# Kernel tuning notes

Measured on AMD Instinct MI355X. Metric: run time of the kernel, lower is better.

## Reference

```python
import jax, jax.numpy as jnp
import numpy as np

N = 1_000_000
D_IN = 9      # 4 (pe) + 1 (q) + 4 (s)
D_H = 30      # dim_evolution
D_OUT = 1     # dim
SLOPE = 0.01  # torch LeakyReLU default negative_slope


def setup_inputs() -> dict:
    key = jax.random.key(0)
    ks = jax.random.split(key, 11)
    def lin(kw, kb, fan_in, fan_out):
        bound = 1.0 / np.sqrt(fan_in)
        W = jax.random.uniform(kw, (fan_in, fan_out), jnp.float32, -bound, bound)
        b = jax.random.uniform(kb, (fan_out,), jnp.float32, -bound, bound)
        return W, b
    W1, b1 = lin(ks[0], ks[1], D_IN, D_H)
    W2, b2 = lin(ks[2], ks[3], D_H, D_H)
    W3, b3 = lin(ks[4], ks[5], D_H, D_H)
    W4, b4 = lin(ks[6], ks[7], D_H, D_OUT)
    return {
        "input_pe": jax.random.normal(ks[8], (N, 4), jnp.float32),
        "input_q": jax.random.normal(ks[9], (N, 1), jnp.float32),
        "input_s": jax.random.normal(ks[10], (N, 4), jnp.float32),
        "W1": W1, "b1": b1, "W2": W2, "b2": b2,
        "W3": W3, "b3": b3, "W4": W4, "b4": b4,
    }


def reference(input_pe, input_q, input_s, W1, b1, W2, b2, W3, b3, W4, b4):
    # forward MLP 9->30->30->30->1 with LeakyReLU
    x = jnp.concatenate([input_pe, input_q, input_s], axis=1)  # [N,9]
    z1 = x @ W1 + b1
    h1 = jnp.where(z1 > 0, z1, SLOPE * z1)
    z2 = h1 @ W2 + b2
    h2 = jnp.where(z2 > 0, z2, SLOPE * z2)
    z3 = h2 @ W3 + b3
    h3 = jnp.where(z3 > 0, z3, SLOPE * z3)
    out = h3 @ W4 + b4  # [N,1]

    # analytic per-sample gradient of scalar output wrt the 9 inputs
    # (equivalent to torch.autograd.grad with grad_outputs=ones)
    gz3 = W4[:, 0][None, :] * jnp.where(z3 > 0, 1.0, SLOPE)  # [N,30]
    gz2 = (gz3 @ W3.T) * jnp.where(z2 > 0, 1.0, SLOPE)       # [N,30]
    gz1 = (gz2 @ W2.T) * jnp.where(z1 > 0, 1.0, SLOPE)       # [N,30]
    gx = gz1 @ W1.T                                           # [N,9]

    n = x.shape[0]
    h_pe = gx[:, 0:4].reshape(n, 1, 4)
    h_q = gx[:, 4:5].reshape(n, 1, 1)
    h_s = gx[:, 5:9].reshape(n, 1, 4)
    return (out, h_s, h_q, h_pe)
```

## Files before the change

kernel.cpp:

```cpp
#include <hip/hip_runtime.h>

#define DH 30
#define SLOPE 0.01f

typedef float v2 __attribute__((ext_vector_type(2)));
#define SB() __builtin_amdgcn_sched_barrier(0)

#define W1_OFF 0
#define W2_OFF 288
#define W3_OFF 1248
#define B1_OFF 2208
#define B2_OFF 2240
#define B3_OFF 2272
#define W4_OFF 2304
#define B4_OFF 2336

__global__ __launch_bounds__(256, 3) void mlp_fwdbwd(
    const float4* __restrict__ pe,
    const float*  __restrict__ q,
    const float4* __restrict__ s,
    const float* __restrict__ W1, const float* __restrict__ b1,
    const float* __restrict__ W2, const float* __restrict__ b2,
    const float* __restrict__ W3, const float* __restrict__ b3,
    const float* __restrict__ W4, const float* __restrict__ b4,
    float* __restrict__ dout, int n)
{
    __shared__ float lw[2368];
    const int tid = threadIdx.x;
    for (int idx = tid; idx < 2368; idx += 256) {
        float v = 0.f;
        if (idx < 288)        { int tt = idx,        r = tt >> 5, c = tt & 31; v = (c < DH) ? W1[r * DH + c] : 0.f; }
        else if (idx < 1248)  { int tt = idx - 288,  r = tt >> 5, c = tt & 31; v = (c < DH) ? W2[r * DH + c] : 0.f; }
        else if (idx < 2208)  { int tt = idx - 1248, r = tt >> 5, c = tt & 31; v = (c < DH) ? W3[r * DH + c] : 0.f; }
        else if (idx < 2240)  { int c = idx - 2208; v = (c < DH) ? b1[c] : 0.f; }
        else if (idx < 2272)  { int c = idx - 2240; v = (c < DH) ? b2[c] : 0.f; }
        else if (idx < 2304)  { int c = idx - 2272; v = (c < DH) ? b3[c] : 0.f; }
        else if (idx < 2336)  { int c = idx - 2304; v = (c < DH) ? W4[c] : 0.f; }
        else if (idx == 2336) { v = b4[0]; }
        lw[idx] = v;
    }
    __syncthreads();

    const int i = blockIdx.x * 256 + tid;
    if (i >= n) return;

    const float4 vpe = pe[i];
    const float4 vs  = s[i];
    const float  vq  = q[i];
    float x[9] = { vpe.x, vpe.y, vpe.z, vpe.w, vq, vs.x, vs.y, vs.z, vs.w };

    v2 acc[15];
    v2 hh[15];
    unsigned m1 = 0, m2 = 0, m3 = 0;
    const v2 slope2 = { SLOPE, SLOPE };

    #define ROW_FMA(OFF, k, sv)                                               \
    {                                                                         \
        const float4* Wr4 = reinterpret_cast<const float4*>(lw + OFF + (k)*32);\
        const v2*     Wr2 = reinterpret_cast<const v2*>(lw + OFF + (k)*32);   \
        _Pragma("unroll")                                                     \
        for (int j4 = 0; j4 < 7; ++j4) {                                      \
            const float4 w = Wr4[j4];                                         \
            const v2 wlo = { w.x, w.y };                                      \
            const v2 whi = { w.z, w.w };                                      \
            acc[2*j4]   = __builtin_elementwise_fma(sv, wlo, acc[2*j4]);      \
            acc[2*j4+1] = __builtin_elementwise_fma(sv, whi, acc[2*j4+1]);    \
        }                                                                     \
        acc[14] = __builtin_elementwise_fma(sv, Wr2[14], acc[14]);            \
    }

    #pragma unroll
    for (int jj = 0; jj < 15; ++jj) acc[jj] = (v2){0.f, 0.f};
    #pragma unroll
    for (int k = 0; k < 9; ++k) {
        const v2 xv = { x[k], x[k] };
        ROW_FMA(W1_OFF, k, xv);
        SB();
    }
    {
        const v2* bv = reinterpret_cast<const v2*>(lw + B1_OFF);
        #pragma unroll
        for (int jj = 0; jj < 15; ++jj) {
            const v2 z = acc[jj] + bv[jj];
            if (z.x > 0.f) m1 |= (1u << (2*jj));
            if (z.y > 0.f) m1 |= (1u << (2*jj+1));
            hh[jj] = __builtin_elementwise_max(z, z * slope2);
        }
    }
    SB();

    #pragma unroll
    for (int jj = 0; jj < 15; ++jj) acc[jj] = (v2){0.f, 0.f};
    #pragma unroll
    for (int k = 0; k < DH; ++k) {
        const float hk = hh[k >> 1][k & 1];
        const v2 hv = { hk, hk };
        ROW_FMA(W2_OFF, k, hv);
        SB();
    }
    {
        const v2* bv = reinterpret_cast<const v2*>(lw + B2_OFF);
        #pragma unroll
        for (int jj = 0; jj < 15; ++jj) {
            const v2 z = acc[jj] + bv[jj];
            if (z.x > 0.f) m2 |= (1u << (2*jj));
            if (z.y > 0.f) m2 |= (1u << (2*jj+1));
            hh[jj] = __builtin_elementwise_max(z, z * slope2);
        }
    }
    SB();

    #pragma unroll
    for (int jj = 0; jj < 15; ++jj) acc[jj] = (v2){0.f, 0.f};
    #pragma unroll
    for (int k = 0; k < DH; ++k) {
        const float hk = hh[k >> 1][k & 1];
        const v2 hv = { hk, hk };
        ROW_FMA(W3_OFF, k, hv);
        SB();
    }
    const float* b3p = lw + B3_OFF;
    const float* W4p = lw + W4_OFF;
    float outv = 0.f;
    #pragma unroll
    for (int j = 0; j < DH; ++j) {
        const float z = acc[j >> 1][j & 1] + b3p[j];
        if (z > 0.f) m3 |= (1u << j);
        const float hz = (z > 0.f) ? z : SLOPE * z;
        outv = fmaf(hz, W4p[j], outv);
    }
    outv += lw[B4_OFF];
    SB();

    v2 g3[15];
    {
        const v2* w4v = reinterpret_cast<const v2*>(W4p);
        #pragma unroll
        for (int jj = 0; jj < 15; ++jj) {
            const v2 w = w4v[jj];
            g3[jj].x = ((m3 >> (2*jj))   & 1u) ? w.x : SLOPE * w.x;
            g3[jj].y = ((m3 >> (2*jj+1)) & 1u) ? w.y : SLOPE * w.y;
        }
    }
    v2 g2[15];
    #pragma unroll
    for (int k = 0; k < DH; k += 2) {
        v2 dA = (v2){0.f, 0.f}, dB = (v2){0.f, 0.f};
        const v2* WrA = reinterpret_cast<const v2*>(W3 + k * DH);
        const v2* WrB = reinterpret_cast<const v2*>(W3 + (k + 1) * DH);
        #pragma unroll
        for (int jj = 0; jj < 15; ++jj) {
            dA = __builtin_elementwise_fma(g3[jj], WrA[jj], dA);
            dB = __builtin_elementwise_fma(g3[jj], WrB[jj], dB);
        }
        const float dotA = dA.x + dA.y;
        const float dotB = dB.x + dB.y;
        g2[k >> 1].x = ((m2 >> k)       & 1u) ? dotA : SLOPE * dotA;
        g2[k >> 1].y = ((m2 >> (k + 1)) & 1u) ? dotB : SLOPE * dotB;
    }
    v2 g1[15];
    #pragma unroll
    for (int k = 0; k < DH; k += 2) {
        v2 dA = (v2){0.f, 0.f}, dB = (v2){0.f, 0.f};
        const v2* WrA = reinterpret_cast<const v2*>(W2 + k * DH);
        const v2* WrB = reinterpret_cast<const v2*>(W2 + (k + 1) * DH);
        #pragma unroll
        for (int jj = 0; jj < 15; ++jj) {
            dA = __builtin_elementwise_fma(g2[jj], WrA[jj], dA);
            dB = __builtin_elementwise_fma(g2[jj], WrB[jj], dB);
        }
        const float dotA = dA.x + dA.y;
        const float dotB = dB.x + dB.y;
        g1[k >> 1].x = ((m1 >> k)       & 1u) ? dotA : SLOPE * dotA;
        g1[k >> 1].y = ((m1 >> (k + 1)) & 1u) ? dotB : SLOPE * dotB;
    }
    float gx[9];
    #pragma unroll
    for (int k = 0; k < 9; ++k) {
        v2 d = (v2){0.f, 0.f};
        const v2* Wr = reinterpret_cast<const v2*>(W1 + k * DH);
        #pragma unroll
        for (int jj = 0; jj < 15; ++jj)
            d = __builtin_elementwise_fma(g1[jj], Wr[jj], d);
        gx[k] = d.x + d.y;
    }

    dout[i] = outv;
    float4* hs = reinterpret_cast<float4*>(dout + (size_t)n);
    hs[i] = make_float4(gx[5], gx[6], gx[7], gx[8]);
    dout[(size_t)5 * n + i] = gx[4];
    float4* hpe = reinterpret_cast<float4*>(dout + (size_t)6 * n);
    hpe[i] = make_float4(gx[0], gx[1], gx[2], gx[3]);
}

extern "C" void kernel_launch(void* const* d_in, const int* in_sizes, int n_in,
                              void* d_out, int out_size, void* d_ws, size_t ws_size,
                              hipStream_t stream) {
    const int n = in_sizes[1];
    const int blocks = (n + 255) / 256;
    hipLaunchKernelGGL(mlp_fwdbwd, dim3(blocks), dim3(256), 0, stream,
        (const float4*)d_in[0], (const float*)d_in[1], (const float4*)d_in[2],
        (const float*)d_in[3], (const float*)d_in[4],
        (const float*)d_in[5], (const float*)d_in[6],
        (const float*)d_in[7], (const float*)d_in[8],
        (const float*)d_in[9], (const float*)d_in[10],
        (float*)d_out, n);
}
```

Baseline: 134.1 us.

## Alternate forward/backward weight sources between LDS and scalar loads by block parity

Even blocks keep the original scheme: the forward pass reads weights from LDS and the backward pass uses uniform global (scalar) loads. Odd blocks swap the two, with the forward pass on scalar loads of the global weights and the backward dot products on LDS. The aim is to spread pressure between the LDS pipe and the scalar/constant cache pipe across co-resident blocks. This roughly doubles code size and may raise register pressure or instruction-cache misses.

```diff
diff --git a/kernel.cpp b/kernel.cpp
--- a/kernel.cpp
+++ b/kernel.cpp
@@ -53,6 +53,8 @@
     v2 hh[15];
     unsigned m1 = 0, m2 = 0, m3 = 0;
     const v2 slope2 = { SLOPE, SLOPE };
+    float outv;
+    float gx[9];
 
     #define ROW_FMA(OFF, k, sv)                                               \
     {                                                                         \
@@ -68,121 +70,232 @@
         }                                                                     \
         acc[14] = __builtin_elementwise_fma(sv, Wr2[14], acc[14]);            \
     }
-
-    #pragma unroll
-    for (int jj = 0; jj < 15; ++jj) acc[jj] = (v2){0.f, 0.f};
-    #pragma unroll
-    for (int k = 0; k < 9; ++k) {
-        const v2 xv = { x[k], x[k] };
-        ROW_FMA(W1_OFF, k, xv);
+    #define ROW_FMA_SM(W, k, sv)                                              \
+    {                                                                         \
+        const v2* Wr = reinterpret_cast<const v2*>(W + (k) * DH);             \
+        _Pragma("unroll")                                                     \
+        for (int jj = 0; jj < 15; ++jj)                                       \
+            acc[jj] = __builtin_elementwise_fma(sv, Wr[jj], acc[jj]);         \
+    }
+    #define ROW_DOT_LDS(OFF, k, G, D)                                         \
+    {                                                                         \
+        const float4* Wr4 = reinterpret_cast<const float4*>(lw + OFF + (k)*32);\
+        const v2*     Wr2 = reinterpret_cast<const v2*>(lw + OFF + (k)*32);   \
+        v2 da = (v2){0.f, 0.f}, db = (v2){0.f, 0.f};                          \
+        _Pragma("unroll")                                                     \
+        for (int j4 = 0; j4 < 7; ++j4) {                                      \
+            const float4 w = Wr4[j4];                                         \
+            const v2 wlo = { w.x, w.y };                                      \
+            const v2 whi = { w.z, w.w };                                      \
+            da = __builtin_elementwise_fma(G[2*j4],   wlo, da);               \
+            db = __builtin_elementwise_fma(G[2*j4+1], whi, db);               \
+        }                                                                     \
+        da = __builtin_elementwise_fma(G[14], Wr2[14], da);                   \
+        D = (da.x + da.y) + (db.x + db.y);                                    \
+    }
+
+    if ((blockIdx.x & 1) == 0) {
+        #pragma unroll
+        for (int jj = 0; jj < 15; ++jj) acc[jj] = (v2){0.f, 0.f};
+        #pragma unroll
+        for (int k = 0; k < 9; ++k) {
+            const v2 xv = { x[k], x[k] };
+            ROW_FMA(W1_OFF, k, xv);
+            SB();
+        }
+        {
+            const v2* bv = reinterpret_cast<const v2*>(lw + B1_OFF);
+            #pragma unroll
+            for (int jj = 0; jj < 15; ++jj) {
+                const v2 z = acc[jj] + bv[jj];
+                if (z.x > 0.f) m1 |= (1u << (2*jj));
+                if (z.y > 0.f) m1 |= (1u << (2*jj+1));
+                hh[jj] = __builtin_elementwise_max(z, z * slope2);
+            }
+        }
         SB();
-    }
-    {
-        const v2* bv = reinterpret_cast<const v2*>(lw + B1_OFF);
-        #pragma unroll
-        for (int jj = 0; jj < 15; ++jj) {
-            const v2 z = acc[jj] + bv[jj];
-            if (z.x > 0.f) m1 |= (1u << (2*jj));
-            if (z.y > 0.f) m1 |= (1u << (2*jj+1));
-            hh[jj] = __builtin_elementwise_max(z, z * slope2);
-        }
-    }
-    SB();
-
-    #pragma unroll
-    for (int jj = 0; jj < 15; ++jj) acc[jj] = (v2){0.f, 0.f};
-    #pragma unroll
-    for (int k = 0; k < DH; ++k) {
-        const float hk = hh[k >> 1][k & 1];
-        const v2 hv = { hk, hk };
-        ROW_FMA(W2_OFF, k, hv);
+        #pragma unroll
+        for (int jj = 0; jj < 15; ++jj) acc[jj] = (v2){0.f, 0.f};
+        #pragma unroll
+        for (int k = 0; k < DH; ++k) {
+            const float hk = hh[k >> 1][k & 1];
+            const v2 hv = { hk, hk };
+            ROW_FMA(W2_OFF, k, hv);
+            SB();
+        }
+        {
+            const v2* bv = reinterpret_cast<const v2*>(lw + B2_OFF);
+            #pragma unroll
+            for (int jj = 0; jj < 15; ++jj) {
+                const v2 z = acc[jj] + bv[jj];
+                if (z.x > 0.f) m2 |= (1u << (2*jj));
+                if (z.y > 0.f) m2 |= (1u << (2*jj+1));
+                hh[jj] = __builtin_elementwise_max(z, z * slope2);
+            }
+        }
         SB();
-    }
-    {
-        const v2* bv = reinterpret_cast<const v2*>(lw + B2_OFF);
-        #pragma unroll
-        for (int jj = 0; jj < 15; ++jj) {
-            const v2 z = acc[jj] + bv[jj];
-            if (z.x > 0.f) m2 |= (1u << (2*jj));
-            if (z.y > 0.f) m2 |= (1u << (2*jj+1));
-            hh[jj] = __builtin_elementwise_max(z, z * slope2);
-        }
-    }
-    SB();
-
-    #pragma unroll
-    for (int jj = 0; jj < 15; ++jj) acc[jj] = (v2){0.f, 0.f};
-    #pragma unroll
-    for (int k = 0; k < DH; ++k) {
-        const float hk = hh[k >> 1][k & 1];
-        const v2 hv = { hk, hk };
-        ROW_FMA(W3_OFF, k, hv);
+        #pragma unroll
+        for (int jj = 0; jj < 15; ++jj) acc[jj] = (v2){0.f, 0.f};
+        #pragma unroll
+        for (int k = 0; k < DH; ++k) {
+            const float hk = hh[k >> 1][k & 1];
+            const v2 hv = { hk, hk };
+            ROW_FMA(W3_OFF, k, hv);
+            SB();
+        }
+        {
+            const float* b3p = lw + B3_OFF;
+            const float* W4p = lw + W4_OFF;
+            outv = 0.f;
+            #pragma unroll
+            for (int j = 0; j < DH; ++j) {
+                const float z = acc[j >> 1][j & 1] + b3p[j];
+                if (z > 0.f) m3 |= (1u << j);
+                const float hz = (z > 0.f) ? z : SLOPE * z;
+                outv = fmaf(hz, W4p[j], outv);
+            }
+            outv += lw[B4_OFF];
+        }
         SB();
-    }
-    const float* b3p = lw + B3_OFF;
-    const float* W4p = lw + W4_OFF;
-    float outv = 0.f;
-    #pragma unroll
-    for (int j = 0; j < DH; ++j) {
-        const float z = acc[j >> 1][j & 1] + b3p[j];
-        if (z > 0.f) m3 |= (1u << j);
-        const float hz = (z > 0.f) ? z : SLOPE * z;
-        outv = fmaf(hz, W4p[j], outv);
-    }
-    outv += lw[B4_OFF];
-    SB();
-
-    v2 g3[15];
-    {
-        const v2* w4v = reinterpret_cast<const v2*>(W4p);
-        #pragma unroll
-        for (int jj = 0; jj < 15; ++jj) {
-            const v2 w = w4v[jj];
-            g3[jj].x = ((m3 >> (2*jj))   & 1u) ? w.x : SLOPE * w.x;
-            g3[jj].y = ((m3 >> (2*jj+1)) & 1u) ? w.y : SLOPE * w.y;
-        }
-    }
-    v2 g2[15];
-    #pragma unroll
-    for (int k = 0; k < DH; k += 2) {
-        v2 dA = (v2){0.f, 0.f}, dB = (v2){0.f, 0.f};
-        const v2* WrA = reinterpret_cast<const v2*>(W3 + k * DH);
-        const v2* WrB = reinterpret_cast<const v2*>(W3 + (k + 1) * DH);
-        #pragma unroll
-        for (int jj = 0; jj < 15; ++jj) {
-            dA = __builtin_elementwise_fma(g3[jj], WrA[jj], dA);
-            dB = __builtin_elementwise_fma(g3[jj], WrB[jj], dB);
-        }
-        const float dotA = dA.x + dA.y;
-        const float dotB = dB.x + dB.y;
-        g2[k >> 1].x = ((m2 >> k)       & 1u) ? dotA : SLOPE * dotA;
-        g2[k >> 1].y = ((m2 >> (k + 1)) & 1u) ? dotB : SLOPE * dotB;
-    }
-    v2 g1[15];
-    #pragma unroll
-    for (int k = 0; k < DH; k += 2) {
-        v2 dA = (v2){0.f, 0.f}, dB = (v2){0.f, 0.f};
-        const v2* WrA = reinterpret_cast<const v2*>(W2 + k * DH);
-        const v2* WrB = reinterpret_cast<const v2*>(W2 + (k + 1) * DH);
-        #pragma unroll
-        for (int jj = 0; jj < 15; ++jj) {
-            dA = __builtin_elementwise_fma(g2[jj], WrA[jj], dA);
-            dB = __builtin_elementwise_fma(g2[jj], WrB[jj], dB);
-        }
-        const float dotA = dA.x + dA.y;
-        const float dotB = dB.x + dB.y;
-        g1[k >> 1].x = ((m1 >> k)       & 1u) ? dotA : SLOPE * dotA;
-        g1[k >> 1].y = ((m1 >> (k + 1)) & 1u) ? dotB : SLOPE * dotB;
-    }
-    float gx[9];
-    #pragma unroll
-    for (int k = 0; k < 9; ++k) {
-        v2 d = (v2){0.f, 0.f};
-        const v2* Wr = reinterpret_cast<const v2*>(W1 + k * DH);
-        #pragma unroll
-        for (int jj = 0; jj < 15; ++jj)
-            d = __builtin_elementwise_fma(g1[jj], Wr[jj], d);
-        gx[k] = d.x + d.y;
+        v2 g3[15];
+        {
+            const v2* w4v = reinterpret_cast<const v2*>(lw + W4_OFF);
+            #pragma unroll
+            for (int jj = 0; jj < 15; ++jj) {
+                const v2 w = w4v[jj];
+                g3[jj].x = ((m3 >> (2*jj))   & 1u) ? w.x : SLOPE * w.x;
+                g3[jj].y = ((m3 >> (2*jj+1)) & 1u) ? w.y : SLOPE * w.y;
+            }
+        }
+        v2 g2[15];
+        #pragma unroll
+        for (int k = 0; k < DH; k += 2) {
+            v2 dA = (v2){0.f, 0.f}, dB = (v2){0.f, 0.f};
+            const v2* WrA = reinterpret_cast<const v2*>(W3 + k * DH);
+            const v2* WrB = reinterpret_cast<const v2*>(W3 + (k + 1) * DH);
+            #pragma unroll
+            for (int jj = 0; jj < 15; ++jj) {
+                dA = __builtin_elementwise_fma(g3[jj], WrA[jj], dA);
+                dB = __builtin_elementwise_fma(g3[jj], WrB[jj], dB);
+            }
+            const float dotA = dA.x + dA.y;
+            const float dotB = dB.x + dB.y;
+            g2[k >> 1].x = ((m2 >> k)       & 1u) ? dotA : SLOPE * dotA;
+            g2[k >> 1].y = ((m2 >> (k + 1)) & 1u) ? dotB : SLOPE * dotB;
+        }
+        v2 g1[15];
+        #pragma unroll
+        for (int k = 0; k < DH; k += 2) {
+            v2 dA = (v2){0.f, 0.f}, dB = (v2){0.f, 0.f};
+            const v2* WrA = reinterpret_cast<const v2*>(W2 + k * DH);
+            const v2* WrB = reinterpret_cast<const v2*>(W2 + (k + 1) * DH);
+            #pragma unroll
+            for (int jj = 0; jj < 15; ++jj) {
+                dA = __builtin_elementwise_fma(g2[jj], WrA[jj], dA);
+                dB = __builtin_elementwise_fma(g2[jj], WrB[jj], dB);
+            }
+            const float dotA = dA.x + dA.y;
+            const float dotB = dB.x + dB.y;
+            g1[k >> 1].x = ((m1 >> k)       & 1u) ? dotA : SLOPE * dotA;
+            g1[k >> 1].y = ((m1 >> (k + 1)) & 1u) ? dotB : SLOPE * dotB;
+        }
+        #pragma unroll
+        for (int k = 0; k < 9; ++k) {
+            v2 d = (v2){0.f, 0.f};
+            const v2* Wr = reinterpret_cast<const v2*>(W1 + k * DH);
+            #pragma unroll
+            for (int jj = 0; jj < 15; ++jj)
+                d = __builtin_elementwise_fma(g1[jj], Wr[jj], d);
+            gx[k] = d.x + d.y;
+        }
+    } else {
+        #pragma unroll
+        for (int jj = 0; jj < 15; ++jj) acc[jj] = (v2){0.f, 0.f};
+        #pragma unroll
+        for (int k = 0; k < 9; ++k) {
+            const v2 xv = { x[k], x[k] };
+            ROW_FMA_SM(W1, k, xv);
+        }
+        {
+            const v2* bv = reinterpret_cast<const v2*>(b1);
+            #pragma unroll
+            for (int jj = 0; jj < 15; ++jj) {
+                const v2 z = acc[jj] + bv[jj];
+                if (z.x > 0.f) m1 |= (1u << (2*jj));
+                if (z.y > 0.f) m1 |= (1u << (2*jj+1));
+                hh[jj] = __builtin_elementwise_max(z, z * slope2);
+            }
+        }
+        #pragma unroll
+        for (int jj = 0; jj < 15; ++jj) acc[jj] = (v2){0.f, 0.f};
+        #pragma unroll
+        for (int k = 0; k < DH; ++k) {
+            const float hk = hh[k >> 1][k & 1];
+            const v2 hv = { hk, hk };
+            ROW_FMA_SM(W2, k, hv);
+        }
+        {
+            const v2* bv = reinterpret_cast<const v2*>(b2);
+            #pragma unroll
+            for (int jj = 0; jj < 15; ++jj) {
+                const v2 z = acc[jj] + bv[jj];
+                if (z.x > 0.f) m2 |= (1u << (2*jj));
+                if (z.y > 0.f) m2 |= (1u << (2*jj+1));
+                hh[jj] = __builtin_elementwise_max(z, z * slope2);
+            }
+        }
+        #pragma unroll
+        for (int jj = 0; jj < 15; ++jj) acc[jj] = (v2){0.f, 0.f};
+        #pragma unroll
+        for (int k = 0; k < DH; ++k) {
+            const float hk = hh[k >> 1][k & 1];
+            const v2 hv = { hk, hk };
+            ROW_FMA_SM(W3, k, hv);
+        }
+        {
+            outv = 0.f;
+            #pragma unroll
+            for (int j = 0; j < DH; ++j) {
+                const float z = acc[j >> 1][j & 1] + b3[j];
+                if (z > 0.f) m3 |= (1u << j);
+                const float hz = (z > 0.f) ? z : SLOPE * z;
+                outv = fmaf(hz, W4[j], outv);
+            }
+            outv += b4[0];
+        }
+        v2 g3[15];
+        {
+            const v2* w4v = reinterpret_cast<const v2*>(lw + W4_OFF);
+            #pragma unroll
+            for (int jj = 0; jj < 15; ++jj) {
+                const v2 w = w4v[jj];
+                g3[jj].x = ((m3 >> (2*jj))   & 1u) ? w.x : SLOPE * w.x;
+                g3[jj].y = ((m3 >> (2*jj+1)) & 1u) ? w.y : SLOPE * w.y;
+            }
+        }
+        v2 g2[15];
+        #pragma unroll
+        for (int k = 0; k < DH; ++k) {
+            float dot;
+            ROW_DOT_LDS(W3_OFF, k, g3, dot);
+            g2[k >> 1][k & 1] = ((m2 >> k) & 1u) ? dot : SLOPE * dot;
+            SB();
+        }
+        v2 g1[15];
+        #pragma unroll
+        for (int k = 0; k < DH; ++k) {
+            float dot;
+            ROW_DOT_LDS(W2_OFF, k, g2, dot);
+            g1[k >> 1][k & 1] = ((m1 >> k) & 1u) ? dot : SLOPE * dot;
+            SB();
+        }
+        #pragma unroll
+        for (int k = 0; k < 9; ++k) {
+            float dot;
+            ROW_DOT_LDS(W1_OFF, k, g1, dot);
+            gx[k] = dot;
+            SB();
+        }
     }
 
     dout[i] = outv;
```

Result: faster. 127.6 us (-4.8%).
